# Optimization experiments

Hardware: AMD Instinct MI355X
Metric: run time of the kernel (lower is better)

## Reference

```python
import jax, jax.numpy as jnp
import numpy as np

N = 100000   # nodes
E = 25000    # hyperedges
M = 640000   # incidence pairs
D = 128      # feature dim (in == out, so no res_linear)
EPS = 1e-5


def setup_inputs() -> dict:
    key = jax.random.key(0)
    ks = jax.random.split(key, 7)
    X = jax.random.normal(ks[0], (N, D), dtype=jnp.float32)
    X0 = jax.random.normal(ks[1], (N, D), dtype=jnp.float32)
    vertex = jax.random.randint(ks[2], (M,), 0, N)
    edges = jax.random.randint(ks[3], (M,), 0, E)
    degE = jax.random.uniform(ks[4], (E, 1), dtype=jnp.float32)
    degV = jax.random.uniform(ks[5], (N, 1), dtype=jnp.float32)
    # xavier-uniform-ish linear weight, no bias
    W = jax.random.normal(ks[6], (D, D), dtype=jnp.float32) * np.float32(1.0 / np.sqrt(D))
    ln_w = jnp.ones((D,), dtype=jnp.float32)
    ln_b = jnp.zeros((D,), dtype=jnp.float32)
    alpha = jnp.asarray(0.1, dtype=jnp.float32)
    beta = jnp.asarray(0.5, dtype=jnp.float32)
    return {"X": X, "X0": X0, "degE": degE, "degV": degV, "W": W,
            "alpha": alpha, "beta": beta, "ln_w": ln_w, "ln_b": ln_b,
            "vertex": vertex, "edges": edges}


def reference(X, X0, degE, degV, W, alpha, beta, ln_w, ln_b, vertex, edges):
    # vertex -> hyperedge aggregation (mean), then degree scale
    Xve = X[vertex]                                          # [M, D]
    esum = jax.ops.segment_sum(Xve, edges, num_segments=E)   # [E, D]
    ecnt = jax.ops.segment_sum(jnp.ones((Xve.shape[0], 1), X.dtype), edges, num_segments=E)
    Xe = (esum / jnp.maximum(ecnt, 1.0)) * degE              # [E, D]
    # hyperedge -> vertex aggregation (sum), degree scale
    Xev = Xe[edges]                                          # [M, D]
    Xv = jax.ops.segment_sum(Xev, vertex, num_segments=N) * degV  # [N, D]
    # residual: in_features == out_features -> residual = Xv itself
    Xh = Xv + Xv
    # LayerNorm over feature dim
    mu = jnp.mean(Xh, axis=-1, keepdims=True)
    var = jnp.mean((Xh - mu) ** 2, axis=-1, keepdims=True)
    Xn = (Xh - mu) * jax.lax.rsqrt(var + EPS) * ln_w + ln_b
    # GCNII combination
    Xi = (1.0 - alpha) * Xn + alpha * X0
    return (1.0 - beta) * Xi + beta * (Xi @ W.T)
```

## Files before the change

### kernel.cpp

```cpp
#include <hip/hip_runtime.h>
#include <hip/hip_fp16.h>
#include <hip/hip_bf16.h>

#define D 128
#define NRR 16
#define NCH 32
#define CVT_BLOCKS 512
#define RE_SL 1600
#define RV_SL 6272

typedef __attribute__((ext_vector_type(8))) short bf16x8;
typedef __attribute__((ext_vector_type(4))) float f32x4;

__device__ __forceinline__ __half2 u2h(unsigned u) { return __builtin_bit_cast(__half2, u); }
__device__ __forceinline__ unsigned pack_h2(float a, float b) {
  __half2 h = __float22half2_rn(make_float2(a, b));
  return __builtin_bit_cast(unsigned, h);
}
__device__ __forceinline__ ushort f2bf(float x) {
  __hip_bfloat16 b = __float2bfloat16(x);
  return __builtin_bit_cast(ushort, b);
}

__global__ __launch_bounds__(512) void count_tab(
    const int* __restrict__ edges, const int* __restrict__ vertex,
    int* __restrict__ T_E, int* __restrict__ T_V, int E, int N, int M,
    const float* __restrict__ X, uint2* __restrict__ Xh,
    const float* __restrict__ X0, uint2* X0h, int do_x0, int xn4) {
  __shared__ int he[RE_SL];
  __shared__ int hv[RV_SL];
  int b = blockIdx.x;
  if (b >= NRR * NCH) {
    const f32x4* X4 = (const f32x4*)X;
    const f32x4* X04 = (const f32x4*)X0;
    int stride = (gridDim.x - NRR * NCH) * 512;
    int lim = do_x0 ? (2 * xn4) : xn4;
    for (int i = (b - NRR * NCH) * 512 + threadIdx.x; i < lim; i += stride) {
      int j = (i < xn4) ? i : (i - xn4);
      f32x4 v = (i < xn4) ? X4[j] : X04[j];
      uint2 o = make_uint2(pack_h2(v[0], v[1]), pack_h2(v[2], v[3]));
      if (i < xn4) Xh[j] = o; else X0h[j] = o;
    }
    return;
  }
  int r = b & (NRR - 1), c = b >> 4;
  int RE = (E + NRR - 1) / NRR, RV = (N + NRR - 1) / NRR;
  int eLo = r * RE, eHi = min(eLo + RE, E);
  int vLo = r * RV, vHi = min(vLo + RV, N);
  int eLen = eHi - eLo, vLen = vHi - vLo;
  for (int i = threadIdx.x; i < eLen; i += 512) he[i] = 0;
  for (int i = threadIdx.x; i < vLen; i += 512) hv[i] = 0;
  __syncthreads();
  const int4* E4 = (const int4*)edges;
  const int4* V4 = (const int4*)vertex;
  int m4 = M >> 2;
  int per = (m4 + NCH - 1) / NCH;
  int i0 = c * per, i1 = min(i0 + per, m4);

#define PROC_CNT(ek, vk)                                               \
  {                                                                    \
    if ((ek).x >= eLo && (ek).x < eHi) atomicAdd(&he[(ek).x - eLo], 1);\
    if ((ek).y >= eLo && (ek).y < eHi) atomicAdd(&he[(ek).y - eLo], 1);\
    if ((ek).z >= eLo && (ek).z < eHi) atomicAdd(&he[(ek).z - eLo], 1);\
    if ((ek).w >= eLo && (ek).w < eHi) atomicAdd(&he[(ek).w - eLo], 1);\
    if ((vk).x >= vLo && (vk).x < vHi) atomicAdd(&hv[(vk).x - vLo], 1);\
    if ((vk).y >= vLo && (vk).y < vHi) atomicAdd(&hv[(vk).y - vLo], 1);\
    if ((vk).z >= vLo && (vk).z < vHi) atomicAdd(&hv[(vk).z - vLo], 1);\
    if ((vk).w >= vLo && (vk).w < vHi) atomicAdd(&hv[(vk).w - vLo], 1);\
  }

  int i = i0 + threadIdx.x;
  for (; i + 1536 < i1; i += 2048) {
    int4 e0 = E4[i], e1 = E4[i + 512], e2 = E4[i + 1024], e3 = E4[i + 1536];
    int4 v0 = V4[i], v1 = V4[i + 512], v2 = V4[i + 1024], v3 = V4[i + 1536];
    PROC_CNT(e0, v0); PROC_CNT(e1, v1); PROC_CNT(e2, v2); PROC_CNT(e3, v3);
  }
  for (; i < i1; i += 512) {
    int4 ek = E4[i];
    int4 vk = V4[i];
    PROC_CNT(ek, vk);
  }
  if (c == NCH - 1) {
    for (int m = (m4 << 2) + threadIdx.x; m < M; m += 512) {
      int e = edges[m], v = vertex[m];
      if (e >= eLo && e < eHi) atomicAdd(&he[e - eLo], 1);
      if (v >= vLo && v < vHi) atomicAdd(&hv[v - vLo], 1);
    }
  }
  __syncthreads();
  for (int i2 = threadIdx.x; i2 < eLen; i2 += 512) T_E[(size_t)c * E + eLo + i2] = he[i2];
  for (int i2 = threadIdx.x; i2 < vLen; i2 += 512) T_V[(size_t)c * N + vLo + i2] = hv[i2];
}

__device__ __forceinline__ int block_exscan(int x, int tid, int* wsum) {
  int lane = tid & 63, w = tid >> 6;
  int v = x;
  #pragma unroll
  for (int off = 1; off < 64; off <<= 1) {
    int t = __shfl_up(v, off);
    if (lane >= off) v += t;
  }
  if (lane == 63) wsum[w] = v;
  __syncthreads();
  if (w == 0 && lane < 16) {
    int s = wsum[lane];
    #pragma unroll
    for (int off = 1; off < 16; off <<= 1) {
      int t = __shfl_up(s, off);
      if (lane >= off) s += t;
    }
    wsum[lane] = s;
  }
  __syncthreads();
  int woff = (w == 0) ? 0 : wsum[w - 1];
  return woff + v - x;
}

__global__ __launch_bounds__(1024) void scan_fused(
    int* __restrict__ T_E, int* __restrict__ C_E, int* __restrict__ A_E, int E,
    int* __restrict__ T_V, int* __restrict__ C_V, int* __restrict__ A_V, int N,
    int* __restrict__ sums, int BE) {
  __shared__ int wsum[16];
  int b = blockIdx.x;
  bool isE = b < BE;
  int* T = isE ? T_E : T_V;
  int* C = isE ? C_E : C_V;
  int* A = isE ? A_E : A_V;
  int len = isE ? E : N;
  int base = (isE ? b : (b - BE)) << 10;
  int id = base + threadIdx.x;
  int run = 0;
  if (id < len) {
    #pragma unroll
    for (int c = 0; c < NCH; ++c) {
      int t = T[(size_t)c * len + id];
      T[(size_t)c * len + id] = run;
      run += t;
    }
    C[id] = run;
  }
  int ex = block_exscan(run, threadIdx.x, wsum);
  if (id < len) A[id] = ex;
  if (threadIdx.x == 0) sums[b] = wsum[15];
}

__global__ __launch_bounds__(1024) void scan_add2(
    int* __restrict__ A_E, int E, int* __restrict__ A_V, int N,
    const int* __restrict__ sums, int BE, int BV,
    const float* __restrict__ W, const float* __restrict__ beta_p,
    ushort* __restrict__ Wbf) {
  int nb = BE + BV;
  if ((int)blockIdx.x >= nb) {
    int idx = (blockIdx.x - nb) * 1024 + threadIdx.x;
    if (idx < D * D) {
      int j = idx >> 7, k = idx & 127;
      float beta = *beta_p;
      float v = beta * W[idx] + ((j == k) ? (1.f - beta) : 0.f);
      Wbf[idx] = f2bf(v);
    }
    return;
  }
  __shared__ int wsum[16];
  __shared__ int pb, pbe;
  int x = ((int)threadIdx.x < nb) ? sums[threadIdx.x] : 0;
  int ex = block_exscan(x, threadIdx.x, wsum);
  if (threadIdx.x == blockIdx.x) pb = ex;
  if ((int)threadIdx.x == BE) pbe = ex;
  __syncthreads();
  bool isE = (int)blockIdx.x < BE;
  int off = isE ? pb : (pb - pbe);
  int* A = isE ? A_E : A_V;
  int len = isE ? E : N;
  int base = (isE ? blockIdx.x : (blockIdx.x - BE)) << 10;
  int i = base + threadIdx.x;
  if (i < len) A[i] += off;
}

__global__ __launch_bounds__(512) void scatter_tab(
    const int* __restrict__ edges, const int* __restrict__ vertex,
    const int* __restrict__ A_E, const int* __restrict__ A_V,
    const int* __restrict__ T_E, const int* __restrict__ T_V,
    int* __restrict__ colE, int* __restrict__ colV, int E, int N, int M) {
  __shared__ int offE[RE_SL];
  __shared__ int curE[RE_SL];
  __shared__ int offV[RV_SL];
  __shared__ int curV[RV_SL];
  int b = blockIdx.x;
  int r = b & (NRR - 1), c = b >> 4;
  int RE = (E + NRR - 1) / NRR, RV = (N + NRR - 1) / NRR;
  int eLo = r * RE, eHi = min(eLo + RE, E);
  int vLo = r * RV, vHi = min(vLo + RV, N);
  int eLen = eHi - eLo, vLen = vHi - vLo;
  for (int i = threadIdx.x; i < eLen; i += 512) {
    offE[i] = A_E[eLo + i] + T_E[(size_t)c * E + eLo + i];
    curE[i] = 0;
  }
  for (int i = threadIdx.x; i < vLen; i += 512) {
    offV[i] = A_V[vLo + i] + T_V[(size_t)c * N + vLo + i];
    curV[i] = 0;
  }
  __syncthreads();
  const int4* E4 = (const int4*)edges;
  const int4* V4 = (const int4*)vertex;
  int m4 = M >> 2;
  int per = (m4 + NCH - 1) / NCH;
  int i0 = c * per, i1 = min(i0 + per, m4);

#define PROC_SCAT(ek, vk)                                                   \
  {                                                                         \
    int es_[4] = {(ek).x, (ek).y, (ek).z, (ek).w};                          \
    int vs_[4] = {(vk).x, (vk).y, (vk).z, (vk).w};                          \
    _Pragma("unroll")                                                       \
    for (int t = 0; t < 4; ++t) {                                           \
      if (es_[t] >= eLo && es_[t] < eHi) {                                  \
        int p2 = atomicAdd(&curE[es_[t] - eLo], 1);                         \
        colE[offE[es_[t] - eLo] + p2] = vs_[t];                             \
      }                                                                     \
      if (vs_[t] >= vLo && vs_[t] < vHi) {                                  \
        int p2 = atomicAdd(&curV[vs_[t] - vLo], 1);                         \
        colV[offV[vs_[t] - vLo] + p2] = es_[t];                             \
      }                                                                     \
    }                                                                       \
  }

  int i = i0 + threadIdx.x;
  for (; i + 512 < i1; i += 1024) {
    int4 ea = E4[i], eb = E4[i + 512];
    int4 va = V4[i], vb = V4[i + 512];
    PROC_SCAT(ea, va);
    PROC_SCAT(eb, vb);
  }
  for (; i < i1; i += 512) {
    int4 ek = E4[i];
    int4 vk = V4[i];
    PROC_SCAT(ek, vk);
  }
  if (c == NCH - 1) {
    for (int m = (m4 << 2) + threadIdx.x; m < M; m += 512) {
      int e = edges[m], v = vertex[m];
      if (e >= eLo && e < eHi) {
        int p = atomicAdd(&curE[e - eLo], 1);
        colE[offE[e - eLo] + p] = v;
      }
      if (v >= vLo && v < vHi) {
        int p = atomicAdd(&curV[v - vLo], 1);
        colV[offV[v - vLo] + p] = e;
      }
    }
  }
}

__global__ __launch_bounds__(256) void edge_agg_q(
    const uint4* __restrict__ Xh4, const float* __restrict__ degE,
    const int* __restrict__ A_E, const int* __restrict__ C_E,
    const int* __restrict__ colE, uint4* __restrict__ Xe4, int E) {
  int ql = threadIdx.x & 15;
  int eid = blockIdx.x * 16 + (threadIdx.x >> 4);
  if (eid >= E) return;
  int s = A_E[eid], cnt = C_E[eid];
  float f0 = 0.f, f1 = 0.f, f2 = 0.f, f3 = 0.f, f4 = 0.f, f5 = 0.f, f6 = 0.f, f7 = 0.f;
  int idx = s, rem = cnt;
  while (rem > 0) {
    int r[16];
    #pragma unroll
    for (int t = 0; t < 16; ++t) r[t] = colE[idx + (t < rem ? t : 0)];
    #pragma unroll
    for (int t = 0; t < 16; ++t) {
      uint4 v = Xh4[(size_t)r[t] * 16 + ql];
      if (t < rem) {
        float2 p0 = __half22float2(u2h(v.x));
        float2 p1 = __half22float2(u2h(v.y));
        float2 p2 = __half22float2(u2h(v.z));
        float2 p3 = __half22float2(u2h(v.w));
        f0 += p0.x; f1 += p0.y; f2 += p1.x; f3 += p1.y;
        f4 += p2.x; f5 += p2.y; f6 += p3.x; f7 += p3.y;
      }
    }
    idx += 16;
    rem -= 16;
  }
  float scale = degE[eid] / fmaxf((float)cnt, 1.0f);
  uint4 o;
  o.x = pack_h2(f0 * scale, f1 * scale);
  o.y = pack_h2(f2 * scale, f3 * scale);
  o.z = pack_h2(f4 * scale, f5 * scale);
  o.w = pack_h2(f6 * scale, f7 * scale);
  Xe4[(size_t)eid * 16 + ql] = o;
}

__global__ __launch_bounds__(256) void vertex_fused(
    const uint4* __restrict__ Xe4, const float* __restrict__ X0,
    const uint4* X0h, int useh,
    const float* __restrict__ degV, const float* __restrict__ ln_w,
    const float* __restrict__ ln_b, const float* __restrict__ alpha_p,
    const int* __restrict__ A_V, const int* __restrict__ C_V,
    const int* __restrict__ colV, const ushort* __restrict__ Wbf,
    float* __restrict__ out, int N) {
  __shared__ __align__(16) ushort XiT[64 * 136];
  int ql = threadIdx.x & 15;
  int grp = threadIdx.x >> 4;
  int n0 = blockIdx.x * 64;
  const f32x4* lw4 = (const f32x4*)ln_w;
  const f32x4* lb4 = (const f32x4*)ln_b;
  f32x4 lwa = lw4[ql * 2], lwb = lw4[ql * 2 + 1];
  f32x4 lba = lb4[ql * 2], lbb = lb4[ql * 2 + 1];
  float alpha = *alpha_p;

  #pragma unroll 1
  for (int p = 0; p < 4; ++p) {
    int r = p * 16 + grp;
    int n = n0 + r;
    uint4 o = make_uint4(0u, 0u, 0u, 0u);
    if (n < N) {
      int s = A_V[n], cnt = C_V[n];
      float f0 = 0.f, f1 = 0.f, f2 = 0.f, f3 = 0.f, f4 = 0.f, f5 = 0.f, f6 = 0.f, f7 = 0.f;
      int idx = s, rem = cnt;
      while (rem > 0) {
        int rr[8];
        #pragma unroll
        for (int t = 0; t < 8; ++t) rr[t] = colV[idx + (t < rem ? t : 0)];
        #pragma unroll
        for (int t = 0; t < 8; ++t) {
          uint4 v = Xe4[(size_t)rr[t] * 16 + ql];
          if (t < rem) {
            float2 p0 = __half22float2(u2h(v.x));
            float2 p1 = __half22float2(u2h(v.y));
            float2 p2 = __half22float2(u2h(v.z));
            float2 p3 = __half22float2(u2h(v.w));
            f0 += p0.x; f1 += p0.y; f2 += p1.x; f3 += p1.y;
            f4 += p2.x; f5 += p2.y; f6 += p3.x; f7 += p3.y;
          }
        }
        idx += 8;
        rem -= 8;
      }
      float sm = ((f0 + f1) + (f2 + f3)) + ((f4 + f5) + (f6 + f7));
      float qq = ((f0 * f0 + f1 * f1) + (f2 * f2 + f3 * f3)) +
                 ((f4 * f4 + f5 * f5) + (f6 * f6 + f7 * f7));
      #pragma unroll
      for (int off = 1; off < 16; off <<= 1) {
        sm += __shfl_xor(sm, off);
        qq += __shfl_xor(qq, off);
      }
      float dv = degV[n];
      float csc = 2.f * dv;
      float mu = csc * sm * (1.f / 128.f);
      float var = csc * csc * qq * (1.f / 128.f) - mu * mu;
      float rstd = rsqrtf(var + 1e-5f);
      float x00[8];
      if (useh) {
        uint4 xh = X0h[(size_t)n * 16 + ql];
        float2 q0 = __half22float2(u2h(xh.x));
        float2 q1 = __half22float2(u2h(xh.y));
        float2 q2 = __half22float2(u2h(xh.z));
        float2 q3 = __half22float2(u2h(xh.w));
        x00[0] = q0.x; x00[1] = q0.y; x00[2] = q1.x; x00[3] = q1.y;
        x00[4] = q2.x; x00[5] = q2.y; x00[6] = q3.x; x00[7] = q3.y;
      } else {
        f32x4 x0a = ((const f32x4*)X0)[(size_t)n * 32 + ql * 2];
        f32x4 x0b = ((const f32x4*)X0)[(size_t)n * 32 + ql * 2 + 1];
        x00[0] = x0a[0]; x00[1] = x0a[1]; x00[2] = x0a[2]; x00[3] = x0a[3];
        x00[4] = x0b[0]; x00[5] = x0b[1]; x00[6] = x0b[2]; x00[7] = x0b[3];
      }
      float ff[8] = {f0, f1, f2, f3, f4, f5, f6, f7};
      float lww[8] = {lwa[0], lwa[1], lwa[2], lwa[3], lwb[0], lwb[1], lwb[2], lwb[3]};
      float lbs[8] = {lba[0], lba[1], lba[2], lba[3], lbb[0], lbb[1], lbb[2], lbb[3]};
      ushort ob[8];
      #pragma unroll
      for (int i = 0; i < 8; ++i) {
        float xhv = csc * ff[i];
        float xn = (xhv - mu) * rstd * lww[i] + lbs[i];
        float xi = (1.f - alpha) * xn + alpha * x00[i];
        ob[i] = f2bf(xi);
      }
      o.x = (unsigned)ob[0] | ((unsigned)ob[1] << 16);
      o.y = (unsigned)ob[2] | ((unsigned)ob[3] << 16);
      o.z = (unsigned)ob[4] | ((unsigned)ob[5] << 16);
      o.w = (unsigned)ob[6] | ((unsigned)ob[7] << 16);
    }
    *(uint4*)(&XiT[r * 136 + ql * 8]) = o;
  }
  __syncthreads();

  int wv = threadIdx.x >> 6, lane = threadIdx.x & 63;
  const bf16x8* W8 = (const bf16x8*)Wbf;
  f32x4 acc[8] = {};
  #pragma unroll
  for (int ks = 0; ks < 4; ++ks) {
    int row = wv * 16 + (lane & 15);
    int slot = ks * 4 + (lane >> 4);
    bf16x8 a = *(const bf16x8*)(&XiT[row * 136 + slot * 8]);
    #pragma unroll
    for (int c = 0; c < 8; ++c) {
      int col = c * 16 + (lane & 15);
      bf16x8 bb = W8[col * 16 + slot];
      acc[c] = __builtin_amdgcn_mfma_f32_16x16x32_bf16(a, bb, acc[c], 0, 0, 0);
    }
  }
  #pragma unroll
  for (int c = 0; c < 8; ++c) {
    #pragma unroll
    for (int i = 0; i < 4; ++i) {
      int row = n0 + wv * 16 + (lane >> 4) * 4 + i;
      int col = c * 16 + (lane & 15);
      if (row < N) out[(size_t)row * 128 + col] = acc[c][i];
    }
  }
}

extern "C" void kernel_launch(void* const* d_in, const int* in_sizes, int n_in,
                              void* d_out, int out_size, void* d_ws, size_t ws_size,
                              hipStream_t stream) {
  const float* X     = (const float*)d_in[0];
  const float* X0    = (const float*)d_in[1];
  const float* degE  = (const float*)d_in[2];
  const float* degV  = (const float*)d_in[3];
  const float* W     = (const float*)d_in[4];
  const float* alpha = (const float*)d_in[5];
  const float* beta  = (const float*)d_in[6];
  const float* lnw   = (const float*)d_in[7];
  const float* lnb   = (const float*)d_in[8];
  const int* vertex  = (const int*)d_in[9];
  const int* edges   = (const int*)d_in[10];

  const int N = in_sizes[0] / D;
  const int E = in_sizes[2];
  const int M = in_sizes[9];

  const int BE = (E + 1023) >> 10;
  const int BV = (N + 1023) >> 10;

  char* p = (char*)d_ws;
  auto alloc = [&](size_t bytes) { char* r = p; p += (bytes + 255) & ~255ull; return r; };
  int* A_E  = (int*)alloc((size_t)E * 4);
  int* A_V  = (int*)alloc((size_t)N * 4);
  int* C_E  = (int*)alloc((size_t)E * 4);
  int* C_V  = (int*)alloc((size_t)N * 4);
  int* sums = (int*)alloc(1024);
  int* colE = (int*)alloc((size_t)M * 4);
  int* colV = (int*)alloc((size_t)M * 4);
  int* T_E  = (int*)alloc((size_t)NCH * E * 4);
  int* T_V  = (int*)alloc((size_t)NCH * N * 4);
  uint2* X_h  = (uint2*)alloc((size_t)N * D * 2);
  uint4* Xe4  = (uint4*)alloc((size_t)E * D * 2);
  ushort* Wbf = (ushort*)alloc(16384 * 2);

  size_t used = (size_t)(p - (char*)d_ws);
  size_t x0h_bytes = ((size_t)N * D * 2 + 255) & ~255ull;
  int do_x0 = (used + x0h_bytes <= ws_size) ? 1 : 0;
  uint2* X0h = do_x0 ? (uint2*)alloc((size_t)N * D * 2) : nullptr;

  count_tab<<<NRR * NCH + CVT_BLOCKS, 512, 0, stream>>>(
      edges, vertex, T_E, T_V, E, N, M, X, X_h, X0, X0h, do_x0, N * D / 4);
  scan_fused<<<BE + BV, 1024, 0, stream>>>(T_E, C_E, A_E, E, T_V, C_V, A_V, N, sums, BE);
  scan_add2<<<BE + BV + 16, 1024, 0, stream>>>(A_E, E, A_V, N, sums, BE, BV, W, beta, Wbf);
  scatter_tab<<<NRR * NCH, 512, 0, stream>>>(edges, vertex, A_E, A_V, T_E, T_V,
                                             colE, colV, E, N, M);
  edge_agg_q<<<(E + 15) / 16, 256, 0, stream>>>((const uint4*)X_h, degE, A_E, C_E,
                                                colE, Xe4, E);
  vertex_fused<<<(N + 63) / 64, 256, 0, stream>>>(
      Xe4, X0, (const uint4*)X0h, do_x0, degV, lnw, lnb, alpha,
      A_V, C_V, colV, Wbf, (float*)d_out, N);
}
```

Measured before the change: 166.5 us.

## Use 1024-thread blocks in vertex_fused, one row per 16-lane group

The vertex kernel now launches 1024 threads per block, so each 16-lane group gathers exactly one of the block's 64 rows instead of looping over four. The 16 waves then split the 4x8 grid of 16x16 MFMA output tiles, two tiles per wave, in place of each wave computing a full 16x128 row strip. The aim is more memory-level parallelism in the latency-bound gather and fewer live accumulator registers per thread. The cost is a heavier block-wide barrier and lower per-thread register limits under the larger launch bound, which may cause spills or limit how many blocks fit per CU.

```diff
diff --git a/kernel.cpp b/kernel.cpp
--- a/kernel.cpp
+++ b/kernel.cpp
@@ -288,7 +288,7 @@
   Xe4[(size_t)eid * 16 + ql] = o;
 }
 
-__global__ __launch_bounds__(256) void vertex_fused(
+__global__ __launch_bounds__(1024) void vertex_fused(
     const uint4* __restrict__ Xe4, const float* __restrict__ X0,
     const uint4* X0h, int useh,
     const float* __restrict__ degV, const float* __restrict__ ln_w,
@@ -300,110 +300,105 @@
   int ql = threadIdx.x & 15;
   int grp = threadIdx.x >> 4;
   int n0 = blockIdx.x * 64;
-  const f32x4* lw4 = (const f32x4*)ln_w;
-  const f32x4* lb4 = (const f32x4*)ln_b;
-  f32x4 lwa = lw4[ql * 2], lwb = lw4[ql * 2 + 1];
-  f32x4 lba = lb4[ql * 2], lbb = lb4[ql * 2 + 1];
-  float alpha = *alpha_p;
-
-  #pragma unroll 1
-  for (int p = 0; p < 4; ++p) {
-    int r = p * 16 + grp;
-    int n = n0 + r;
-    uint4 o = make_uint4(0u, 0u, 0u, 0u);
-    if (n < N) {
-      int s = A_V[n], cnt = C_V[n];
-      float f0 = 0.f, f1 = 0.f, f2 = 0.f, f3 = 0.f, f4 = 0.f, f5 = 0.f, f6 = 0.f, f7 = 0.f;
-      int idx = s, rem = cnt;
-      while (rem > 0) {
-        int rr[8];
-        #pragma unroll
-        for (int t = 0; t < 8; ++t) rr[t] = colV[idx + (t < rem ? t : 0)];
-        #pragma unroll
-        for (int t = 0; t < 8; ++t) {
-          uint4 v = Xe4[(size_t)rr[t] * 16 + ql];
-          if (t < rem) {
-            float2 p0 = __half22float2(u2h(v.x));
-            float2 p1 = __half22float2(u2h(v.y));
-            float2 p2 = __half22float2(u2h(v.z));
-            float2 p3 = __half22float2(u2h(v.w));
-            f0 += p0.x; f1 += p0.y; f2 += p1.x; f3 += p1.y;
-            f4 += p2.x; f5 += p2.y; f6 += p3.x; f7 += p3.y;
-          }
+  int n = n0 + grp;
+
+  uint4 o = make_uint4(0u, 0u, 0u, 0u);
+  if (n < N) {
+    const f32x4* lw4 = (const f32x4*)ln_w;
+    const f32x4* lb4 = (const f32x4*)ln_b;
+    f32x4 lwa = lw4[ql * 2], lwb = lw4[ql * 2 + 1];
+    f32x4 lba = lb4[ql * 2], lbb = lb4[ql * 2 + 1];
+    float alpha = *alpha_p;
+    int s = A_V[n], cnt = C_V[n];
+    float f0 = 0.f, f1 = 0.f, f2 = 0.f, f3 = 0.f, f4 = 0.f, f5 = 0.f, f6 = 0.f, f7 = 0.f;
+    int idx = s, rem = cnt;
+    while (rem > 0) {
+      int rr[8];
+      #pragma unroll
+      for (int t = 0; t < 8; ++t) rr[t] = colV[idx + (t < rem ? t : 0)];
+      #pragma unroll
+      for (int t = 0; t < 8; ++t) {
+        uint4 v = Xe4[(size_t)rr[t] * 16 + ql];
+        if (t < rem) {
+          float2 p0 = __half22float2(u2h(v.x));
+          float2 p1 = __half22float2(u2h(v.y));
+          float2 p2 = __half22float2(u2h(v.z));
+          float2 p3 = __half22float2(u2h(v.w));
+          f0 += p0.x; f1 += p0.y; f2 += p1.x; f3 += p1.y;
+          f4 += p2.x; f5 += p2.y; f6 += p3.x; f7 += p3.y;
         }
-        idx += 8;
-        rem -= 8;
       }
-      float sm = ((f0 + f1) + (f2 + f3)) + ((f4 + f5) + (f6 + f7));
-      float qq = ((f0 * f0 + f1 * f1) + (f2 * f2 + f3 * f3)) +
-                 ((f4 * f4 + f5 * f5) + (f6 * f6 + f7 * f7));
-      #pragma unroll
-      for (int off = 1; off < 16; off <<= 1) {
-        sm += __shfl_xor(sm, off);
-        qq += __shfl_xor(qq, off);
-      }
-      float dv = degV[n];
-      float csc = 2.f * dv;
-      float mu = csc * sm * (1.f / 128.f);
-      float var = csc * csc * qq * (1.f / 128.f) - mu * mu;
-      float rstd = rsqrtf(var + 1e-5f);
-      float x00[8];
-      if (useh) {
-        uint4 xh = X0h[(size_t)n * 16 + ql];
-        float2 q0 = __half22float2(u2h(xh.x));
-        float2 q1 = __half22float2(u2h(xh.y));
-        float2 q2 = __half22float2(u2h(xh.z));
-        float2 q3 = __half22float2(u2h(xh.w));
-        x00[0] = q0.x; x00[1] = q0.y; x00[2] = q1.x; x00[3] = q1.y;
-        x00[4] = q2.x; x00[5] = q2.y; x00[6] = q3.x; x00[7] = q3.y;
-      } else {
-        f32x4 x0a = ((const f32x4*)X0)[(size_t)n * 32 + ql * 2];
-        f32x4 x0b = ((const f32x4*)X0)[(size_t)n * 32 + ql * 2 + 1];
-        x00[0] = x0a[0]; x00[1] = x0a[1]; x00[2] = x0a[2]; x00[3] = x0a[3];
-        x00[4] = x0b[0]; x00[5] = x0b[1]; x00[6] = x0b[2]; x00[7] = x0b[3];
-      }
-      float ff[8] = {f0, f1, f2, f3, f4, f5, f6, f7};
-      float lww[8] = {lwa[0], lwa[1], lwa[2], lwa[3], lwb[0], lwb[1], lwb[2], lwb[3]};
-      float lbs[8] = {lba[0], lba[1], lba[2], lba[3], lbb[0], lbb[1], lbb[2], lbb[3]};
-      ushort ob[8];
-      #pragma unroll
-      for (int i = 0; i < 8; ++i) {
-        float xhv = csc * ff[i];
-        float xn = (xhv - mu) * rstd * lww[i] + lbs[i];
-        float xi = (1.f - alpha) * xn + alpha * x00[i];
-        ob[i] = f2bf(xi);
-      }
-      o.x = (unsigned)ob[0] | ((unsigned)ob[1] << 16);
-      o.y = (unsigned)ob[2] | ((unsigned)ob[3] << 16);
-      o.z = (unsigned)ob[4] | ((unsigned)ob[5] << 16);
-      o.w = (unsigned)ob[6] | ((unsigned)ob[7] << 16);
-    }
-    *(uint4*)(&XiT[r * 136 + ql * 8]) = o;
-  }
+      idx += 8;
+      rem -= 8;
+    }
+    float sm = ((f0 + f1) + (f2 + f3)) + ((f4 + f5) + (f6 + f7));
+    float qq = ((f0 * f0 + f1 * f1) + (f2 * f2 + f3 * f3)) +
+               ((f4 * f4 + f5 * f5) + (f6 * f6 + f7 * f7));
+    #pragma unroll
+    for (int off = 1; off < 16; off <<= 1) {
+      sm += __shfl_xor(sm, off);
+      qq += __shfl_xor(qq, off);
+    }
+    float dv = degV[n];
+    float csc = 2.f * dv;
+    float mu = csc * sm * (1.f / 128.f);
+    float var = csc * csc * qq * (1.f / 128.f) - mu * mu;
+    float rstd = rsqrtf(var + 1e-5f);
+    float x00[8];
+    if (useh) {
+      uint4 xh = X0h[(size_t)n * 16 + ql];
+      float2 q0 = __half22float2(u2h(xh.x));
+      float2 q1 = __half22float2(u2h(xh.y));
+      float2 q2 = __half22float2(u2h(xh.z));
+      float2 q3 = __half22float2(u2h(xh.w));
+      x00[0] = q0.x; x00[1] = q0.y; x00[2] = q1.x; x00[3] = q1.y;
+      x00[4] = q2.x; x00[5] = q2.y; x00[6] = q3.x; x00[7] = q3.y;
+    } else {
+      f32x4 x0a = ((const f32x4*)X0)[(size_t)n * 32 + ql * 2];
+      f32x4 x0b = ((const f32x4*)X0)[(size_t)n * 32 + ql * 2 + 1];
+      x00[0] = x0a[0]; x00[1] = x0a[1]; x00[2] = x0a[2]; x00[3] = x0a[3];
+      x00[4] = x0b[0]; x00[5] = x0b[1]; x00[6] = x0b[2]; x00[7] = x0b[3];
+    }
+    float ff[8] = {f0, f1, f2, f3, f4, f5, f6, f7};
+    float lww[8] = {lwa[0], lwa[1], lwa[2], lwa[3], lwb[0], lwb[1], lwb[2], lwb[3]};
+    float lbs[8] = {lba[0], lba[1], lba[2], lba[3], lbb[0], lbb[1], lbb[2], lbb[3]};
+    ushort ob[8];
+    #pragma unroll
+    for (int i = 0; i < 8; ++i) {
+      float xhv = csc * ff[i];
+      float xn = (xhv - mu) * rstd * lww[i] + lbs[i];
+      float xi = (1.f - alpha) * xn + alpha * x00[i];
+      ob[i] = f2bf(xi);
+    }
+    o.x = (unsigned)ob[0] | ((unsigned)ob[1] << 16);
+    o.y = (unsigned)ob[2] | ((unsigned)ob[3] << 16);
+    o.z = (unsigned)ob[4] | ((unsigned)ob[5] << 16);
+    o.w = (unsigned)ob[6] | ((unsigned)ob[7] << 16);
+  }
+  *(uint4*)(&XiT[grp * 136 + ql * 8]) = o;
   __syncthreads();
 
   int wv = threadIdx.x >> 6, lane = threadIdx.x & 63;
   const bf16x8* W8 = (const bf16x8*)Wbf;
-  f32x4 acc[8] = {};
   #pragma unroll
-  for (int ks = 0; ks < 4; ++ks) {
-    int row = wv * 16 + (lane & 15);
-    int slot = ks * 4 + (lane >> 4);
-    bf16x8 a = *(const bf16x8*)(&XiT[row * 136 + slot * 8]);
-    #pragma unroll
-    for (int c = 0; c < 8; ++c) {
-      int col = c * 16 + (lane & 15);
-      bf16x8 bb = W8[col * 16 + slot];
-      acc[c] = __builtin_amdgcn_mfma_f32_16x16x32_bf16(a, bb, acc[c], 0, 0, 0);
-    }
-  }
-  #pragma unroll
-  for (int c = 0; c < 8; ++c) {
+  for (int tt = 0; tt < 2; ++tt) {
+    int tile = wv * 2 + tt;
+    int rt = tile >> 3;
+    int ct = tile & 7;
+    f32x4 acc = {};
+    #pragma unroll
+    for (int ks = 0; ks < 4; ++ks) {
+      int row = rt * 16 + (lane & 15);
+      int slot = ks * 4 + (lane >> 4);
+      bf16x8 a = *(const bf16x8*)(&XiT[row * 136 + slot * 8]);
+      bf16x8 bb = W8[(ct * 16 + (lane & 15)) * 16 + slot];
+      acc = __builtin_amdgcn_mfma_f32_16x16x32_bf16(a, bb, acc, 0, 0, 0);
+    }
     #pragma unroll
     for (int i = 0; i < 4; ++i) {
-      int row = n0 + wv * 16 + (lane >> 4) * 4 + i;
-      int col = c * 16 + (lane & 15);
-      if (row < N) out[(size_t)row * 128 + col] = acc[c][i];
+      int row = n0 + rt * 16 + (lane >> 4) * 4 + i;
+      int col = ct * 16 + (lane & 15);
+      if (row < N) out[(size_t)row * 128 + col] = acc[i];
     }
   }
 }
@@ -458,7 +453,7 @@
                                              colE, colV, E, N, M);
   edge_agg_q<<<(E + 15) / 16, 256, 0, stream>>>((const uint4*)X_h, degE, A_E, C_E,
                                                 colE, Xe4, E);
-  vertex_fused<<<(N + 63) / 64, 256, 0, stream>>>(
+  vertex_fused<<<(N + 63) / 64, 1024, 0, stream>>>(
       Xe4, X0, (const uint4*)X0h, do_x0, degV, lnw, lnb, alpha,
       A_V, C_V, colV, Wbf, (float*)d_out, N);
 }
```

New measurement: 171.0 us. 1.03x slower.
